# Performance work log

Measured on AMD Instinct MI355X. Metric: run time of the kernel, lower is better.

The kernel has to match this reference:

```python
import jax, jax.numpy as jnp
import numpy as np

CAP = 6.0
EPS = 1e-5

def _layernorm(x, g, b):
    mu = jnp.mean(x, axis=-1, keepdims=True)
    var = jnp.mean(jnp.square(x - mu), axis=-1, keepdims=True)
    return (x - mu) * jax.lax.rsqrt(var + EPS) * g + b

def setup_inputs() -> dict:
    key = jax.random.key(0)
    B, S, D, H = 4, 1024, 1024, 16
    DF = int(D * 2.0)
    ks = jax.random.split(key, 8)
    inp = {
        "x": jax.random.normal(ks[0], (B, S, D), dtype=jnp.float32),
        "mask": jnp.tril(jnp.ones((S, S), dtype=bool)),  # causal block mask
        "qkv_w": jax.random.normal(ks[1], (3 * D, D), dtype=jnp.float32) * 0.02,
        "qkv_b": jnp.zeros((3 * D,), dtype=jnp.float32),
        "out_w": jax.random.normal(ks[2], (D, D), dtype=jnp.float32) * 0.02,
        "out_b": jnp.zeros((D,), dtype=jnp.float32),
        "ln1_g": jnp.ones((D,), dtype=jnp.float32),
        "ln1_b": jnp.zeros((D,), dtype=jnp.float32),
        "ln2_g": jnp.ones((D,), dtype=jnp.float32),
        "ln2_b": jnp.zeros((D,), dtype=jnp.float32),
        "ff1_w": jax.random.normal(ks[3], (DF, D), dtype=jnp.float32) * 0.02,
        "ff1_b": jnp.zeros((DF,), dtype=jnp.float32),
        "ff2_w": jax.random.normal(ks[4], (D, DF), dtype=jnp.float32) * 0.02,
        "ff2_b": jnp.zeros((D,), dtype=jnp.float32),
    }
    return inp

def reference(x, mask, qkv_w, qkv_b, out_w, out_b, ln1_g, ln1_b, ln2_g, ln2_b,
              ff1_w, ff1_b, ff2_w, ff2_b):
    B, S, D = x.shape
    H = 16
    dh = D // H
    res = x
    h = _layernorm(x, ln1_g, ln1_b)
    qkv = h @ qkv_w.T + qkv_b                       # [B,S,3D]
    qkv = qkv.reshape(B, S, 3, H, dh).transpose(2, 0, 3, 1, 4)  # [3,B,H,S,dh]
    q, k, v = qkv[0], qkv[1], qkv[2]
    scores = jnp.einsum('bhqd,bhkd->bhqk', q, k) / jnp.sqrt(jnp.float32(dh))
    scores = CAP * jnp.tanh(scores / CAP)            # logit soft-cap score_mod
    scores = jnp.where(mask, scores, jnp.float32(-1e9))
    attn = jax.nn.softmax(scores, axis=-1)
    o = jnp.einsum('bhqk,bhkd->bhqd', attn, v)       # [B,H,S,dh]
    o = o.transpose(0, 2, 1, 3).reshape(B, S, D)
    x = res + (o @ out_w.T + out_b)
    h2 = _layernorm(x, ln2_g, ln2_b)
    ff = jax.nn.gelu(h2 @ ff1_w.T + ff1_b, approximate=False) @ ff2_w.T + ff2_b
    return x + ff
```

## Files before the change

### kernel.cpp

```cpp
#include <hip/hip_runtime.h>
#include <hip/hip_bf16.h>
#include <cmath>

#define NROWS 4096
#define DM    1024

typedef unsigned short u16;
typedef __attribute__((ext_vector_type(8))) short short8;
typedef __attribute__((ext_vector_type(4))) float floatx4;

#if __has_builtin(__builtin_amdgcn_exp2f)
#define EXP2F(x) __builtin_amdgcn_exp2f(x)
#else
#define EXP2F(x) exp2f(x)
#endif
#if __has_builtin(__builtin_amdgcn_rcpf)
#define RCPF(x) __builtin_amdgcn_rcpf(x)
#else
#define RCPF(x) (1.0f / (x))
#endif

__device__ __forceinline__ u16 f2bf(float f) {
    unsigned int u = __float_as_uint(f);
    return (u16)((u + 0x7fffu + ((u >> 16) & 1u)) >> 16);
}

__device__ __forceinline__ void gl_lds16(const u16* g, u16* l) {
    __builtin_amdgcn_global_load_lds(
        (const __attribute__((address_space(1))) unsigned int*)g,
        (__attribute__((address_space(3))) unsigned int*)l, 16, 0, 0);
}

__device__ __forceinline__ size_t pk_off(int row, int k, int KB) {
    const int rt = row >> 6, i = (row >> 4) & 3, lr = row & 15;
    const int kb = k >> 6, s = (k >> 5) & 1, lq = (k >> 3) & 3, j = k & 7;
    return ((((size_t)(rt * KB + kb) * 2 + s) * 4 + i) * 64 + lq * 16 + lr) * 8 + j;
}

__global__ __launch_bounds__(256) void castln_kernel(
    const float* __restrict__ s0, const float* __restrict__ s1,
    const float* __restrict__ s2, const float* __restrict__ s3,
    u16* __restrict__ d0, u16* __restrict__ d1,
    u16* __restrict__ d2, u16* __restrict__ d3,
    const float* __restrict__ x, const float* __restrict__ g,
    const float* __restrict__ beta, u16* __restrict__ hout)
{
    const int bid = blockIdx.x;
    if (bid < 8192) {
        const float* s; u16* d; int base, kbits, KB;
        if (bid < 3072)      { s = s0; d = d0; base = bid;        kbits = 10; KB = 16; }
        else if (bid < 4096) { s = s1; d = d1; base = bid - 3072; kbits = 10; KB = 16; }
        else if (bid < 6144) { s = s2; d = d2; base = bid - 4096; kbits = 10; KB = 16; }
        else                 { s = s3; d = d3; base = bid - 6144; kbits = 11; KB = 32; }
        const int idx = (base * 256 + threadIdx.x) * 4;
        const float4 v = *(const float4*)(s + idx);
        const int row = idx >> kbits, k = idx & ((1 << kbits) - 1);
        *(ushort4*)(d + pk_off(row, k, KB)) =
            make_ushort4(f2bf(v.x), f2bf(v.y), f2bf(v.z), f2bf(v.w));
        return;
    }
    const int row = bid - 8192;
    const int t = threadIdx.x;
    const float4 v = ((const float4*)(x + (size_t)row * DM))[t];
    float s = v.x + v.y + v.z + v.w;
    #pragma unroll
    for (int off = 32; off > 0; off >>= 1) s += __shfl_xor(s, off);
    __shared__ float red[4];
    const int wid = t >> 6;
    if ((t & 63) == 0) red[wid] = s;
    __syncthreads();
    const float mean = (red[0] + red[1] + red[2] + red[3]) * (1.0f / DM);
    const float dx = v.x - mean, dy = v.y - mean, dz = v.z - mean, dw = v.w - mean;
    float ss = dx*dx + dy*dy + dz*dz + dw*dw;
    #pragma unroll
    for (int off = 32; off > 0; off >>= 1) ss += __shfl_xor(ss, off);
    __syncthreads();
    if ((t & 63) == 0) red[wid] = ss;
    __syncthreads();
    const float var = (red[0] + red[1] + red[2] + red[3]) * (1.0f / DM);
    const float rstd = rsqrtf(var + 1e-5f);
    const float4 gv = ((const float4*)g)[t];
    const float4 bv = ((const float4*)beta)[t];
    *(ushort4*)(hout + pk_off(row, t * 4, 16)) = make_ushort4(
        f2bf(dx * rstd * gv.x + bv.x), f2bf(dy * rstd * gv.y + bv.y),
        f2bf(dz * rstd * gv.z + bv.z), f2bf(dw * rstd * gv.w + bv.w));
}

__global__ __launch_bounds__(256) void ln_kernel(
    const float* __restrict__ x, const float* __restrict__ g,
    const float* __restrict__ beta, u16* __restrict__ out)
{
    const int row = blockIdx.x;
    const int t = threadIdx.x;
    const float4 v = ((const float4*)(x + (size_t)row * DM))[t];
    float s = v.x + v.y + v.z + v.w;
    #pragma unroll
    for (int off = 32; off > 0; off >>= 1) s += __shfl_xor(s, off);
    __shared__ float red[4];
    const int wid = t >> 6;
    if ((t & 63) == 0) red[wid] = s;
    __syncthreads();
    const float mean = (red[0] + red[1] + red[2] + red[3]) * (1.0f / DM);
    const float dx = v.x - mean, dy = v.y - mean, dz = v.z - mean, dw = v.w - mean;
    float ss = dx*dx + dy*dy + dz*dz + dw*dw;
    #pragma unroll
    for (int off = 32; off > 0; off >>= 1) ss += __shfl_xor(ss, off);
    __syncthreads();
    if ((t & 63) == 0) red[wid] = ss;
    __syncthreads();
    const float var = (red[0] + red[1] + red[2] + red[3]) * (1.0f / DM);
    const float rstd = rsqrtf(var + 1e-5f);
    const float4 gv = ((const float4*)g)[t];
    const float4 bv = ((const float4*)beta)[t];
    *(ushort4*)(out + pk_off(row, t * 4, 16)) = make_ushort4(
        f2bf(dx * rstd * gv.x + bv.x), f2bf(dy * rstd * gv.y + bv.y),
        f2bf(dz * rstd * gv.z + bv.z), f2bf(dw * rstd * gv.w + bv.w));
}

__device__ __forceinline__ float gelu_f(float v) {
    return 0.5f * v * (1.0f + erff(v * 0.70710678118654752f));
}

template <int ACT, int OUTMODE, int TM>
__global__ __launch_bounds__(256, TM == 128 ? 3 : 4) void gemm_pk_kernel(
    const u16* __restrict__ A, const u16* __restrict__ W,
    const float* __restrict__ bias, const float* __restrict__ res,
    void* __restrict__ Cout, u16* __restrict__ vpout, u16* __restrict__ kpout,
    int N, int K)
{
    constexpr int MI = TM / 32;
    constexpr int NCH = (TM == 128) ? 4 : 3;
    constexpr int STAGEB = NCH * 8192;
    constexpr int EPIB = (OUTMODE == 1) ? 34816 : 17408;
    constexpr int SMEMB = (STAGEB > EPIB) ? STAGEB : EPIB;
    __shared__ __align__(16) char smem[SMEMB];
    u16* St = (u16*)smem;
    float* Cs = (float*)smem;

    const int tid = threadIdx.x;
    const int w = tid >> 6, l = tid & 63;
    const int lr = l & 15, lq = l >> 4;
    const int wm = w >> 1, wn = w & 1;

    const int fid = blockIdx.x;
    const int NB = (N >> 7) >> 3;
    const int xcd = fid & 7;
    const int kk = fid >> 3;
    constexpr int MT_BITS = (TM == 128) ? 5 : 6;
    constexpr int MT_MASK = (1 << MT_BITS) - 1;
    const int nt = xcd * NB + (kk >> MT_BITS);
    const int mt = kk & MT_MASK;
    const int m0 = mt * TM, n0 = nt * 128;
    const int KB = K >> 6;

    const u16* gch[NCH];
    if (TM == 128) {
        gch[0] = A + (size_t)(mt * 2 + 0) * KB * 4096;
        gch[1] = A + (size_t)(mt * 2 + 1) * KB * 4096;
        gch[2] = W + (size_t)(nt * 2 + 0) * KB * 4096;
        gch[3] = W + (size_t)(nt * 2 + 1) * KB * 4096;
    } else {
        gch[0] = A + (size_t)mt * KB * 4096;
        gch[1] = W + (size_t)(nt * 2 + 0) * KB * 4096;
        gch[2] = W + (size_t)(nt * 2 + 1) * KB * 4096;
    }

    floatx4 acc[MI][4] = {};

    auto STAGE = [&](int kb) {
        #pragma unroll
        for (int c = 0; c < NCH; c++) {
            const u16* src = gch[c] + (size_t)kb * 4096 + w * 512 + l * 8;
            u16* ld = St + c * 4096 + w * 512;
            gl_lds16(src, ld);
            gl_lds16(src + 2048, ld + 2048);
        }
    };

    auto COMPUTE = [&]() {
        #pragma unroll
        for (int ts = 0; ts < 2; ts++) {
            short8 af[MI], bf[4];
            #pragma unroll
            for (int i = 0; i < MI; i++) {
                const int off = (TM == 128) ? (wm * 4096 + ts * 2048 + i * 512)
                                            : (ts * 2048 + (wm * 2 + i) * 512);
                af[i] = *(const short8*)(St + off + l * 8);
            }
            constexpr int BB = (TM == 128) ? 2 : 1;
            #pragma unroll
            for (int j = 0; j < 4; j++)
                bf[j] = *(const short8*)(St + (BB + wn) * 4096 + ts * 2048 + j * 512 + l * 8);
            #pragma unroll
            for (int i = 0; i < MI; i++)
                #pragma unroll
                for (int j = 0; j < 4; j++)
                    acc[i][j] = __builtin_amdgcn_mfma_f32_16x16x32_bf16(af[i], bf[j], acc[i][j], 0, 0, 0);
        }
    };

    const int NKB = K >> 6;
    for (int kb = 0; kb < NKB; kb++) {
        STAGE(kb);
        __syncthreads();
        COMPUTE();
        __syncthreads();
    }

    if (OUTMODE == 1) {
        short* Ts = (short*)smem;
        float bj[4];
        #pragma unroll
        for (int j = 0; j < 4; j++) bj[j] = bias[n0 + wn * 64 + j * 16 + lr];
        const bool isV = (n0 >= 2048);
        if (isV) {
            #pragma unroll
            for (int i = 0; i < 4; i++)
                #pragma unroll
                for (int j = 0; j < 4; j++) {
                    const int vcol_l = wn * 64 + j * 16 + lr;
                    const int sbase = wm * 64 + i * 16 + lq * 4;
                    #pragma unroll
                    for (int rp = 0; rp < 2; rp++) {
                        const unsigned pkv =
                            (unsigned)f2bf(acc[i][j][rp * 2] + bj[j]) |
                            ((unsigned)f2bf(acc[i][j][rp * 2 + 1] + bj[j]) << 16);
                        *(unsigned*)&Ts[vcol_l * 136 + sbase + rp * 2] = pkv;
                    }
                }
        } else {
            #pragma unroll
            for (int i = 0; i < 4; i++)
                #pragma unroll
                for (int j = 0; j < 4; j++)
                    #pragma unroll
                    for (int r = 0; r < 4; r++) {
                        const int row_l = wm * 64 + i * 16 + lq * 4 + r;
                        const int col_l = wn * 64 + j * 16 + lr;
                        Ts[row_l * 136 + col_l] = (short)f2bf(acc[i][j][r] + bj[j]);
                    }
        }
        __syncthreads();
        u16* dbuf = isV ? vpout : (n0 >= 1024 ? kpout : (u16*)Cout);
        const int hbase = (n0 & 1023) >> 6;
        const int l0 = (tid * 2) & 63, subp = tid >> 6, sp = (tid >> 5) & 1;
        #pragma unroll
        for (int tl = 0; tl < 2; tl++) {
            const int mg = m0 + tl * 64;
            const int bb2 = mg >> 10, ktile = (mg & 1023) >> 6;
            #pragma unroll
            for (int hl = 0; hl < 2; hl++) {
                const int hh = hbase + hl;
                u16* dst = dbuf + ((size_t)(bb2 * 16 + hh) * 16 + ktile) * 4096 + tid * 16;
                #pragma unroll
                for (int half = 0; half < 2; half++) {
                    const int ll = l0 + half;
                    short8 seg;
                    if (isV) {
                        const int vcol_l = hl * 64 + subp * 16 + (ll & 15);
                        const int srow = tl * 64 + sp * 32 + ((ll >> 4) & 3) * 8;
                        seg = *(const short8*)&Ts[vcol_l * 136 + srow];
                    } else {
                        const int row_l = tl * 64 + subp * 16 + (ll & 15);
                        const int col_l = hl * 64 + sp * 32 + ((ll >> 4) & 3) * 8;
                        seg = *(const short8*)&Ts[row_l * 136 + col_l];
                    }
                    *(short8*)(dst + half * 8) = seg;
                }
            }
        }
        return;
    }

    #pragma unroll
    for (int i = 0; i < MI; i++) {
        __syncthreads();
        #pragma unroll
        for (int r = 0; r < 4; r++) {
            const int rl = wm * 16 + lq * 4 + r;
            #pragma unroll
            for (int j = 0; j < 4; j++)
                Cs[rl * 136 + wn * 64 + j * 16 + lr] = acc[i][j][r];
        }
        __syncthreads();
        #pragma unroll
        for (int q = 0; q < 2; q++) {
            const int s2 = tid * 2 + q;
            const int rid = s2 >> 4, c8 = s2 & 15;
            const int rr = m0 + (rid >> 4) * (TM / 2) + i * 16 + (rid & 15);
            const int col = c8 * 8;
            float vv[8];
            const float4 v0 = *(const float4*)&Cs[rid * 136 + col];
            const float4 v1 = *(const float4*)&Cs[rid * 136 + col + 4];
            const float4 ba = *(const float4*)&bias[n0 + col];
            const float4 bb4 = *(const float4*)&bias[n0 + col + 4];
            vv[0] = v0.x + ba.x;  vv[1] = v0.y + ba.y;  vv[2] = v0.z + ba.z;  vv[3] = v0.w + ba.w;
            vv[4] = v1.x + bb4.x; vv[5] = v1.y + bb4.y; vv[6] = v1.z + bb4.z; vv[7] = v1.w + bb4.w;
            if (ACT) {
                #pragma unroll
                for (int e = 0; e < 8; e++) vv[e] = gelu_f(vv[e]);
            }
            if (OUTMODE == 0) {
                const size_t o0 = (size_t)rr * N + n0 + col;
                if (res) {
                    const float4 r0 = *(const float4*)&res[o0];
                    const float4 r1 = *(const float4*)&res[o0 + 4];
                    vv[0]+=r0.x; vv[1]+=r0.y; vv[2]+=r0.z; vv[3]+=r0.w;
                    vv[4]+=r1.x; vv[5]+=r1.y; vv[6]+=r1.z; vv[7]+=r1.w;
                }
                *(float4*)((float*)Cout + o0)     = make_float4(vv[0], vv[1], vv[2], vv[3]);
                *(float4*)((float*)Cout + o0 + 4) = make_float4(vv[4], vv[5], vv[6], vv[7]);
            } else {
                short8 ov;
                #pragma unroll
                for (int e = 0; e < 8; e++) ov[e] = (short)f2bf(vv[e]);
                *(short8*)((u16*)Cout + pk_off(rr, n0 + col, N >> 6)) = ov;
            }
        }
    }
}

__global__ __launch_bounds__(256, 3) void attn_mfma_kernel(
    const u16* __restrict__ qp, const u16* __restrict__ kp,
    const u16* __restrict__ vp, u16* __restrict__ o)
{
    __shared__ __align__(16) short Ps[4][1152];
    __shared__ __align__(16) short Os[4096];

    const int qt = 15 - blockIdx.y;
    const int bh = blockIdx.x;
    const int b = bh >> 4, h = bh & 15;
    const int tid = threadIdx.x;
    const int w = tid >> 6, l = tid & 63;
    const int C = l & 15, Qd = l >> 4;

    const float C1f = 0.0601122935f, C2f = -17.3123404907f;

    const size_t headoff = (size_t)(b * 16 + h) * 16 * 4096;
    const u16* qb = qp + headoff + (size_t)qt * 4096 + w * 1024 + l * 8;
    const u16* kb = kp + headoff + l * 8;
    const u16* vb = vp + headoff + l * 8;

    short8 qf[2];
    qf[0] = *(const short8*)qb;
    qf[1] = *(const short8*)(qb + 512);

    float l_i = 0.f;
    floatx4 oacc[4] = {};

    short8 kf[8];
    #pragma unroll
    for (int i = 0; i < 8; i++) kf[i] = *(const short8*)(kb + i * 512);

    for (int kt = 0; kt <= qt; kt++) {
        const u16* vv_ = vb + (size_t)kt * 4096;
        short8 vf[8];
        #pragma unroll
        for (int j = 0; j < 8; j++) vf[j] = *(const short8*)(vv_ + j * 512);

        floatx4 sacc[4] = {};
        #pragma unroll
        for (int mt = 0; mt < 4; mt++)
            #pragma unroll
            for (int s = 0; s < 2; s++)
                sacc[mt] = __builtin_amdgcn_mfma_f32_16x16x32_bf16(kf[mt * 2 + s], qf[s], sacc[mt], 0, 0, 0);

        if (kt < qt) {
            const u16* kn_ = kb + (size_t)(kt + 1) * 4096;
            #pragma unroll
            for (int i = 0; i < 8; i++) kf[i] = *(const short8*)(kn_ + i * 512);
        }

        float p[16];
        float rs = 0.f;
        const bool diag = (kt == qt);
        const int qrow = qt * 64 + w * 16 + C;
        #pragma unroll
        for (int mt = 0; mt < 4; mt++)
            #pragma unroll
            for (int r = 0; r < 4; r++) {
                const float e = EXP2F(sacc[mt][r] * C1f);
                float pv = EXP2F(C2f * RCPF(e + 1.0f));
                if (diag) {
                    const int krow = kt * 64 + mt * 16 + Qd * 4 + r;
                    if (krow > qrow) pv = 0.f;
                }
                p[mt * 4 + r] = pv;
                rs += pv;
            }
        rs += __shfl_xor(rs, 16);
        rs += __shfl_xor(rs, 32);
        l_i += rs;

        #pragma unroll
        for (int mt = 0; mt < 4; mt++)
            #pragma unroll
            for (int pr = 0; pr < 2; pr++) {
                union { __hip_bfloat162 b2; unsigned u; } cv;
                cv.b2 = __float22bfloat162_rn(
                    make_float2(p[mt * 4 + pr * 2], p[mt * 4 + pr * 2 + 1]));
                *(unsigned*)&Ps[w][C * 72 + mt * 16 + Qd * 4 + pr * 2] = cv.u;
            }
        short8 pf[2];
        pf[0] = *(const short8*)&Ps[w][C * 72 + Qd * 8];
        pf[1] = *(const short8*)&Ps[w][C * 72 + 32 + Qd * 8];

        #pragma unroll
        for (int dt = 0; dt < 4; dt++)
            #pragma unroll
            for (int s = 0; s < 2; s++)
                oacc[dt] = __builtin_amdgcn_mfma_f32_16x16x32_bf16(pf[s], vf[dt * 2 + s], oacc[dt], 0, 0, 0);
    }

    float linv[4];
    #pragma unroll
    for (int r = 0; r < 4; r++) linv[r] = RCPF(__shfl(l_i, Qd * 4 + r));
    #pragma unroll
    for (int dt = 0; dt < 4; dt++) {
        const int s = dt >> 1;
        const int lqp = (dt & 1) * 2 + (C >> 3);
        const int jj = C & 7;
        #pragma unroll
        for (int r = 0; r < 4; r++)
            Os[((s * 4 + w) * 64 + lqp * 16 + Qd * 4 + r) * 8 + jj] =
                (short)f2bf(oacc[dt][r] * linv[r]);
    }
    __syncthreads();
    u16* obase = o + (size_t)((b * 16 + qt) * 16 + h) * 4096 + tid * 16;
    *(short8*)obase       = *(const short8*)&Os[tid * 16];
    *(short8*)(obase + 8) = *(const short8*)&Os[tid * 16 + 8];
}

extern "C" void kernel_launch(void* const* d_in, const int* in_sizes, int n_in,
                              void* d_out, int out_size, void* d_ws, size_t ws_size,
                              hipStream_t stream)
{
    (void)in_sizes; (void)n_in; (void)out_size; (void)ws_size;
    const float* x     = (const float*)d_in[0];
    const float* qkv_w = (const float*)d_in[2];
    const float* qkv_b = (const float*)d_in[3];
    const float* out_w = (const float*)d_in[4];
    const float* out_b = (const float*)d_in[5];
    const float* ln1_g = (const float*)d_in[6];
    const float* ln1_b = (const float*)d_in[7];
    const float* ln2_g = (const float*)d_in[8];
    const float* ln2_b = (const float*)d_in[9];
    const float* ff1_w = (const float*)d_in[10];
    const float* ff1_b = (const float*)d_in[11];
    const float* ff2_w = (const float*)d_in[12];
    const float* ff2_b = (const float*)d_in[13];
    float* out = (float*)d_out;

    u16* qpbuf = (u16*)d_ws;
    u16* kpbuf = qpbuf + 4194304;
    u16* vpbuf = kpbuf + 4194304;
    u16* hbuf  = (u16*)((char*)d_ws + 33554432);
    u16* obuf  = (u16*)((char*)d_ws + 41943040);
    u16* wq    = (u16*)((char*)d_ws + 50331648);
    u16* wo = wq + 3145728;
    u16* w1 = wo + 1048576;
    u16* w2 = w1 + 2097152;
    u16* ff1buf = (u16*)d_ws;

    castln_kernel<<<12288, 256, 0, stream>>>(
        qkv_w, out_w, ff1_w, ff2_w, wq, wo, w1, w2, x, ln1_g, ln1_b, hbuf);
    gemm_pk_kernel<0,1,128><<<768, 256, 0, stream>>>(
        hbuf, wq, qkv_b, nullptr, qpbuf, vpbuf, kpbuf, 3072, 1024);
    attn_mfma_kernel<<<dim3(64, 16), 256, 0, stream>>>(qpbuf, kpbuf, vpbuf, obuf);
    gemm_pk_kernel<0,0,64><<<512, 256, 0, stream>>>(
        obuf, wo, out_b, x, out, nullptr, nullptr, 1024, 1024);
    ln_kernel<<<NROWS, 256, 0, stream>>>(out, ln2_g, ln2_b, hbuf);
    gemm_pk_kernel<1,2,128><<<512, 256, 0, stream>>>(
        hbuf, w1, ff1_b, nullptr, ff1buf, nullptr, nullptr, 2048, 1024);
    gemm_pk_kernel<0,0,64><<<512, 256, 0, stream>>>(
        ff1buf, w2, ff2_b, out, out, nullptr, nullptr, 1024, 2048);
}
```

Baseline: 278.3 us.

## Stage K/V tiles through double-buffered LDS shared across attention waves

Each of the four waves used to load the full K and V tiles from global memory into its own registers. Now the waves cooperatively copy each 64-row K/V tile into LDS with direct global-to-LDS loads, double-buffered so the next tile is fetched while the current one is computed, and every wave reads its fragments from LDS. This cuts redundant global/L2 traffic by four but adds 32KB of LDS and a block barrier per key tile, which may reduce occupancy under the launch bound of 3 blocks.

```diff
diff --git a/kernel.cpp b/kernel.cpp
--- a/kernel.cpp
+++ b/kernel.cpp
@@ -326,6 +326,8 @@
 {
     __shared__ __align__(16) short Ps[4][1152];
     __shared__ __align__(16) short Os[4096];
+    __shared__ __align__(16) u16 Kl[2][4096];
+    __shared__ __align__(16) u16 Vl[2][4096];
 
     const int qt = 15 - blockIdx.y;
     const int bh = blockIdx.x;
@@ -338,8 +340,8 @@
 
     const size_t headoff = (size_t)(b * 16 + h) * 16 * 4096;
     const u16* qb = qp + headoff + (size_t)qt * 4096 + w * 1024 + l * 8;
-    const u16* kb = kp + headoff + l * 8;
-    const u16* vb = vp + headoff + l * 8;
+    const u16* kb = kp + headoff;
+    const u16* vb = vp + headoff;
 
     short8 qf[2];
     qf[0] = *(const short8*)qb;
@@ -348,15 +350,29 @@
     float l_i = 0.f;
     floatx4 oacc[4] = {};
 
-    short8 kf[8];
-    #pragma unroll
-    for (int i = 0; i < 8; i++) kf[i] = *(const short8*)(kb + i * 512);
+    auto STAGEKV = [&](int kt, int buf) {
+        const u16* ks = kb + (size_t)kt * 4096 + (w * 2) * 512 + l * 8;
+        const u16* vs = vb + (size_t)kt * 4096 + (w * 2) * 512 + l * 8;
+        u16* kd = &Kl[buf][(w * 2) * 512];
+        u16* vd = &Vl[buf][(w * 2) * 512];
+        gl_lds16(ks, kd);
+        gl_lds16(ks + 512, kd + 512);
+        gl_lds16(vs, vd);
+        gl_lds16(vs + 512, vd + 512);
+    };
+
+    int cur = 0;
+    STAGEKV(0, 0);
+    __syncthreads();
 
     for (int kt = 0; kt <= qt; kt++) {
-        const u16* vv_ = vb + (size_t)kt * 4096;
-        short8 vf[8];
-        #pragma unroll
-        for (int j = 0; j < 8; j++) vf[j] = *(const short8*)(vv_ + j * 512);
+        if (kt < qt) STAGEKV(kt + 1, cur ^ 1);
+
+        const u16* Kc = &Kl[cur][0];
+        const u16* Vc = &Vl[cur][0];
+        short8 kf[8];
+        #pragma unroll
+        for (int i = 0; i < 8; i++) kf[i] = *(const short8*)(Kc + i * 512 + l * 8);
 
         floatx4 sacc[4] = {};
         #pragma unroll
@@ -364,12 +380,6 @@
             #pragma unroll
             for (int s = 0; s < 2; s++)
                 sacc[mt] = __builtin_amdgcn_mfma_f32_16x16x32_bf16(kf[mt * 2 + s], qf[s], sacc[mt], 0, 0, 0);
-
-        if (kt < qt) {
-            const u16* kn_ = kb + (size_t)(kt + 1) * 4096;
-            #pragma unroll
-            for (int i = 0; i < 8; i++) kf[i] = *(const short8*)(kn_ + i * 512);
-        }
 
         float p[16];
         float rs = 0.f;
@@ -405,11 +415,18 @@
         pf[0] = *(const short8*)&Ps[w][C * 72 + Qd * 8];
         pf[1] = *(const short8*)&Ps[w][C * 72 + 32 + Qd * 8];
 
+        short8 vf[8];
+        #pragma unroll
+        for (int j = 0; j < 8; j++) vf[j] = *(const short8*)(Vc + j * 512 + l * 8);
+
         #pragma unroll
         for (int dt = 0; dt < 4; dt++)
             #pragma unroll
             for (int s = 0; s < 2; s++)
                 oacc[dt] = __builtin_amdgcn_mfma_f32_16x16x32_bf16(pf[s], vf[dt * 2 + s], oacc[dt], 0, 0, 0);
+
+        __syncthreads();
+        cur ^= 1;
     }
 
     float linv[4];
```

New measurement: 275.2 us. No clear change (-1.1%).
